# Performance work log

Hardware: AMD Instinct MI355X
Metric: run time of the kernel (lower is better)

The kernel has to match this reference:

```python
import jax, jax.numpy as jnp
import numpy as np

B, S, DM, H, D = 4, 2048, 1024, 16, 64
CAP = 15.0
EPS = 1e-6


def setup_inputs() -> dict:
    key = jax.random.key(0)
    ks = jax.random.split(key, 5)
    return {
        "x": jax.random.normal(ks[0], (B, S, DM), jnp.float32),
        "hidden_state": jnp.zeros((B, H, D, D), jnp.float32),
        "w_qkv": jax.random.normal(ks[1], (3 * H * D, DM), jnp.float32) * 0.02,
        "w_gate": jax.random.normal(ks[2], (3 * H, DM), jnp.float32) * 0.02,
        "w_out": jax.random.normal(ks[3], (DM, H * D), jnp.float32) * 0.02,
        "ln_w": jnp.ones((DM,), jnp.float32),
    }


def reference(x, hidden_state, w_qkv, w_gate, w_out, ln_w):
    Bq, Sq, DMq = x.shape
    residual = x
    # RMSNorm (computed in float32, matching the torch module)
    xf = x.astype(jnp.float32)
    var = jnp.mean(xf * xf, axis=-1, keepdims=True)
    xn = ln_w * (xf * jax.lax.rsqrt(var + EPS)).astype(x.dtype)
    # Fused qkv projection: (B,S,3,H,D)
    qkv = jnp.einsum('bsd,od->bso', xn, w_qkv).reshape(Bq, Sq, 3, H, D)
    q, k, v = qkv[:, :, 0], qkv[:, :, 1], qkv[:, :, 2]
    # Gates: (B,S,3,H) -> soft cap -> sigmoid
    gates = jnp.einsum('bsd,od->bso', xn, w_gate).reshape(Bq, Sq, 3, H)
    gates = jax.nn.sigmoid(CAP * jnp.tanh(gates / CAP))
    ig, fg, og = gates[:, :, 0], gates[:, :, 1], gates[:, :, 2]

    def step(h, inp):
        q_t, k_t, v_t, i_t, f_t, o_t = inp  # q/k/v: (B,H,D); gates: (B,H)
        kv = jnp.einsum('bhd,bhe->bhde', k_t, v_t)
        h = f_t[..., None, None] * h + i_t[..., None, None] * kv
        out = o_t[..., None] * jnp.einsum('bhd,bhde->bhe', q_t, h)
        return h, out

    xs = (q.swapaxes(0, 1), k.swapaxes(0, 1), v.swapaxes(0, 1),
          ig.swapaxes(0, 1), fg.swapaxes(0, 1), og.swapaxes(0, 1))
    h_final, outs = jax.lax.scan(step, hidden_state, xs)  # outs: (S,B,H,D)
    output = outs.swapaxes(0, 1).reshape(Bq, Sq, H * D)
    y = residual + output @ w_out.T
    return y, h_final
```

## Files before the change

### kernel.cpp

```cpp
#include <hip/hip_runtime.h>
#include <hip/hip_bf16.h>
#include <math.h>
#include <stdint.h>

#define Bq 4
#define Sq 2048
#define DMq 1024
#define Hq 16
#define Dq 64
#define CAPf 15.0f
#define EPSf 1e-6f
#define Tc 64
#define Cc (Sq / Tc)
#define QKVW (3 * Hq * Dq)

typedef __attribute__((ext_vector_type(8))) short short8;
typedef __attribute__((ext_vector_type(4))) float f32x4;
typedef __hip_bfloat16 bf16;

__device__ __forceinline__ float b2f(bf16 v) { return __bfloat162float(v); }
__device__ __forceinline__ bf16  f2b(float v) { return __float2bfloat16(v); }
__device__ __forceinline__ uint16_t f2bu(float f) {
    bf16 h = __float2bfloat16(f); uint16_t u; __builtin_memcpy(&u, &h, 2); return u;
}
__device__ __forceinline__ float bu2f(uint16_t u) {
    uint32_t x = ((uint32_t)u) << 16; float f; __builtin_memcpy(&f, &x, 4); return f;
}

__global__ void convert_f32_bf16(const float* __restrict__ in, bf16* __restrict__ out, int n4) {
    int i = blockIdx.x * 256 + threadIdx.x;
    if (i < n4) {
        float4 v = ((const float4*)in)[i];
        bf16 t[4] = {f2b(v.x), f2b(v.y), f2b(v.z), f2b(v.w)};
        ((uint2*)out)[i] = *(uint2*)t;
    }
}

__global__ void rmsnorm_kernel(const float* __restrict__ x,
                               const float* __restrict__ ln_w,
                               bf16* __restrict__ xn) {
    int row = blockIdx.x;
    const float4* xr = (const float4*)(x + (size_t)row * DMq);
    int tid = threadIdx.x;
    float4 v = xr[tid];
    float ss = v.x*v.x + v.y*v.y + v.z*v.z + v.w*v.w;
    #pragma unroll
    for (int off = 32; off > 0; off >>= 1) ss += __shfl_down(ss, off);
    __shared__ float red[4];
    int lane = tid & 63, wv = tid >> 6;
    if (lane == 0) red[wv] = ss;
    __syncthreads();
    float tot = red[0] + red[1] + red[2] + red[3];
    float rs = rsqrtf(tot * (1.0f / DMq) + EPSf);
    float4 w4 = ((const float4*)ln_w)[tid];
    bf16 t[4] = {f2b(v.x * rs * w4.x), f2b(v.y * rs * w4.y),
                 f2b(v.z * rs * w4.z), f2b(v.w * rs * w4.w)};
    *(uint2*)(xn + (size_t)row * DMq + tid * 4) = *(uint2*)t;
}

enum Epi { EPI_BF16 = 0, EPI_GATE = 1, EPI_RESID = 2 };

template<int EPI>
__global__ __launch_bounds__(256) void gemm_mfma(const bf16* __restrict__ A,
                                                 const bf16* __restrict__ Bw,
                                                 const float* __restrict__ resid,
                                                 void* __restrict__ Cv,
                                                 int M, int N, int K) {
    __shared__ bf16 As[128 * 64];
    __shared__ bf16 Bs[128 * 64];
    const int tid = threadIdx.x;
    const int w = tid >> 6;
    const int l = tid & 63;
    const int wr = (w >> 1) * 64;
    const int wc = (w & 1) * 64;
    const int bm = blockIdx.y * 128;
    const int bn = blockIdx.x * 128;

    const int lrow = l >> 3;
    const int swzc = ((l & 7) ^ lrow) * 8;

    const int fl = l & 15;
    const int kb = l >> 4;
    const int rsw = l & 7;

    f32x4 acc[4][4];
    #pragma unroll
    for (int i = 0; i < 4; i++)
        #pragma unroll
        for (int j = 0; j < 4; j++) acc[i][j] = (f32x4){0.f, 0.f, 0.f, 0.f};

    for (int k0 = 0; k0 < K; k0 += 64) {
        __syncthreads();
        #pragma unroll
        for (int inst = 0; inst < 4; inst++) {
            int r0 = w * 32 + inst * 8;
            const bf16* gp = A + (size_t)(bm + r0 + lrow) * K + k0 + swzc;
            __builtin_amdgcn_global_load_lds(
                (const __attribute__((address_space(1))) uint32_t*)gp,
                (__attribute__((address_space(3))) uint32_t*)(As + r0 * 64),
                16, 0, 0);
        }
        #pragma unroll
        for (int inst = 0; inst < 4; inst++) {
            int r0 = w * 32 + inst * 8;
            if (bn + r0 < N) {
                const bf16* gp = Bw + (size_t)(bn + r0 + lrow) * K + k0 + swzc;
                __builtin_amdgcn_global_load_lds(
                    (const __attribute__((address_space(1))) uint32_t*)gp,
                    (__attribute__((address_space(3))) uint32_t*)(Bs + r0 * 64),
                    16, 0, 0);
            }
        }
        __syncthreads();
        #pragma unroll
        for (int kk2 = 0; kk2 < 2; kk2++) {
            const int koff = (((kk2 << 2) + kb) ^ rsw) * 8;
            short8 af[4], bfr[4];
            #pragma unroll
            for (int i = 0; i < 4; i++)
                af[i] = *(const short8*)(As + (wr + i * 16 + fl) * 64 + koff);
            #pragma unroll
            for (int j = 0; j < 4; j++)
                bfr[j] = *(const short8*)(Bs + (wc + j * 16 + fl) * 64 + koff);
            #pragma unroll
            for (int i = 0; i < 4; i++)
                #pragma unroll
                for (int j = 0; j < 4; j++)
                    acc[i][j] = __builtin_amdgcn_mfma_f32_16x16x32_bf16(
                        af[i], bfr[j], acc[i][j], 0, 0, 0);
        }
    }

    #pragma unroll
    for (int i = 0; i < 4; i++) {
        #pragma unroll
        for (int j = 0; j < 4; j++) {
            int col = bn + wc + j * 16 + fl;
            if (EPI == EPI_GATE && col >= N) continue;
            #pragma unroll
            for (int r = 0; r < 4; r++) {
                int row = bm + wr + i * 16 + kb * 4 + r;
                size_t idx = (size_t)row * N + col;
                float v = acc[i][j][r];
                if (EPI == EPI_GATE) {
                    v = CAPf * tanhf(v * (1.0f / CAPf));
                    ((float*)Cv)[idx] = 1.0f / (1.0f + expf(-v));
                } else if (EPI == EPI_RESID) {
                    ((float*)Cv)[idx] = v + resid[idx];
                } else {
                    ((bf16*)Cv)[idx] = f2b(v);
                }
            }
        }
    }
}

__global__ __launch_bounds__(64) void chunk_intra(const bf16* __restrict__ qkvb,
                                                  const float* __restrict__ gates,
                                                  bf16* __restrict__ attb,
                                                  bf16* __restrict__ LT,
                                                  float* __restrict__ oaArr,
                                                  float* __restrict__ Fch) {
    const int blk = blockIdx.x;
    const int c  = blk & (Cc - 1);
    const int bh = blk >> 5;
    const int b = bh >> 4, hh = bh & 15;
    const int l = threadIdx.x;
    const int s0 = c * Tc;

    __shared__ bf16 KTs[4096];
    __shared__ bf16 VTs[4096];
    __shared__ bf16 Ps[4096];
    __shared__ float rowS[64], pcolS[64], wstS[64];

    const float* gp = gates + (size_t)(b * Sq + s0 + l) * (3 * Hq);
    float ig = gp[hh], fg = gp[Hq + hh], og = gp[2 * Hq + hh];
    float la = __logf(fg);
    #pragma unroll
    for (int off = 1; off < 64; off <<= 1) {
        float v = __shfl_up(la, off);
        if (l >= off) la += v;
    }
    float la63 = __shfl(la, 63);
    float li = __logf(ig);
    rowS[l]  = la + __logf(og);
    pcolS[l] = li - la;
    wstS[l]  = __expf(la63 - la + li);
    float oa = og * __expf(la);
    oaArr[(size_t)blk * 64 + l] = oa;
    if (l == 0) Fch[blk] = __expf(la63);
    __syncthreads();

    const int cg = l & 7, rp = l >> 3;
    const size_t rowBase = (size_t)(b * Sq + s0);
    const int kcol = (Hq + hh) * Dq, vcol = (2 * Hq + hh) * Dq;
    #pragma unroll
    for (int pass = 0; pass < 4; pass++) {
        int j0 = pass * 16 + rp * 2;
        const bf16* r0 = qkvb + (rowBase + j0) * QKVW;
        const bf16* r1 = qkvb + (rowBase + j0 + 1) * QKVW;
        short8 k0 = *(const short8*)(r0 + kcol + cg * 8);
        short8 k1 = *(const short8*)(r1 + kcol + cg * 8);
        short8 v0 = *(const short8*)(r0 + vcol + cg * 8);
        short8 v1 = *(const short8*)(r1 + vcol + cg * 8);
        float w0 = wstS[j0], w1 = wstS[j0 + 1];
        #pragma unroll
        for (int s = 0; s < 8; s++) {
            int cc = cg * 8 + s;
            int base = cc * 64 + ((((j0 >> 3) ^ (cc & 7) ^ (cc >> 3))) << 3) + (j0 & 7);
            uint32_t kp = (uint32_t)f2bu(bu2f((uint16_t)k0[s]) * w0)
                        | ((uint32_t)f2bu(bu2f((uint16_t)k1[s]) * w1) << 16);
            uint32_t vp = (uint32_t)(uint16_t)v0[s] | ((uint32_t)(uint16_t)v1[s] << 16);
            *(uint32_t*)&KTs[base] = kp;
            *(uint32_t*)&VTs[base] = vp;
        }
    }

    const int fl = l & 15, kb = l >> 4;
    const bf16* Qb = qkvb + rowBase * QKVW + hh * Dq;
    const bf16* Kb = qkvb + rowBase * QKVW + kcol;
    f32x4 accS[4][4];
    #pragma unroll
    for (int i = 0; i < 4; i++)
        #pragma unroll
        for (int j = 0; j < 4; j++) accS[i][j] = (f32x4){0.f, 0.f, 0.f, 0.f};
    #pragma unroll
    for (int ks = 0; ks < 2; ks++) {
        short8 qf[4], kf[4];
        #pragma unroll
        for (int i = 0; i < 4; i++)
            qf[i] = *(const short8*)(Qb + (size_t)(i * 16 + fl) * QKVW + ks * 32 + kb * 8);
        #pragma unroll
        for (int j = 0; j < 4; j++)
            kf[j] = *(const short8*)(Kb + (size_t)(j * 16 + fl) * QKVW + ks * 32 + kb * 8);
        #pragma unroll
        for (int i = 0; i < 4; i++)
            #pragma unroll
            for (int j = 0; j < 4; j++)
                accS[i][j] = __builtin_amdgcn_mfma_f32_16x16x32_bf16(qf[i], kf[j], accS[i][j], 0, 0, 0);
    }

    #pragma unroll
    for (int i = 0; i < 4; i++) {
        #pragma unroll
        for (int j = 0; j < 4; j++) {
            int jj = j * 16 + fl;
            float pc = pcolS[jj];
            #pragma unroll
            for (int r = 0; r < 4; r++) {
                int t = i * 16 + kb * 4 + r;
                float p = (jj <= t) ? __expf(rowS[t] + pc) * accS[i][j][r] : 0.f;
                int slot = (jj >> 3) ^ (t & 7) ^ (t >> 3);
                Ps[t * 64 + slot * 8 + (jj & 7)] = f2b(p);
            }
        }
    }
    __syncthreads();

    f32x4 accO[4][4], accL[4][4];
    #pragma unroll
    for (int i = 0; i < 4; i++)
        #pragma unroll
        for (int j = 0; j < 4; j++) {
            accO[i][j] = (f32x4){0.f, 0.f, 0.f, 0.f};
            accL[i][j] = (f32x4){0.f, 0.f, 0.f, 0.f};
        }
    #pragma unroll
    for (int ks = 0; ks < 2; ks++) {
        short8 pf[4], vt[4], kt[4];
        #pragma unroll
        for (int i = 0; i < 4; i++) {
            int row = i * 16 + fl;
            int koff = (((ks * 4 + kb) ^ (row & 7) ^ (row >> 3))) << 3;
            pf[i] = *(const short8*)(Ps  + row * 64 + koff);
            vt[i] = *(const short8*)(VTs + row * 64 + koff);
            kt[i] = *(const short8*)(KTs + row * 64 + koff);
        }
        #pragma unroll
        for (int i = 0; i < 4; i++)
            #pragma unroll
            for (int j = 0; j < 4; j++) {
                accO[i][j] = __builtin_amdgcn_mfma_f32_16x16x32_bf16(pf[i], vt[j], accO[i][j], 0, 0, 0);
                accL[i][j] = __builtin_amdgcn_mfma_f32_16x16x32_bf16(vt[i], kt[j], accL[i][j], 0, 0, 0);
            }
    }

    #pragma unroll
    for (int i = 0; i < 4; i++)
        #pragma unroll
        for (int j = 0; j < 4; j++)
            #pragma unroll
            for (int r = 0; r < 4; r++) {
                int rr = i * 16 + kb * 4 + r, cc2 = j * 16 + fl;
                attb[(rowBase + rr) * (Hq * Dq) + hh * Dq + cc2] = f2b(accO[i][j][r]);
                LT[(size_t)blk * 4096 + rr * 64 + cc2] = f2b(accL[i][j][r]);
            }
}

__global__ __launch_bounds__(256) void scan_pass2(bf16* __restrict__ LH,
                                                  const float* __restrict__ Fchunk,
                                                  const float* __restrict__ h0,
                                                  float* __restrict__ hfin) {
    int idx = blockIdx.x * 256 + threadIdx.x;
    int bh = idx >> 12;
    int ed = idx & 4095;
    int e = ed >> 6, d = ed & 63;
    float run = h0[(size_t)bh * 4096 + d * 64 + e];
    #pragma unroll
    for (int c = 0; c < Cc; c++) {
        float Fv = Fchunk[bh * Cc + c];
        size_t off = ((size_t)bh * Cc + c) * 4096 + ed;
        float Lv = b2f(LH[off]);
        LH[off] = f2b(run);
        run = Fv * run + Lv;
    }
    hfin[(size_t)bh * 4096 + d * 64 + e] = run;
}

__global__ __launch_bounds__(64) void chunk_cross(const bf16* __restrict__ qkvb,
                                                  const bf16* __restrict__ HT,
                                                  const float* __restrict__ oaArr,
                                                  bf16* __restrict__ attb) {
    const int blk = blockIdx.x;
    const int c = blk & (Cc - 1);
    const int bh = blk >> 5;
    const int b = bh >> 4, hh = bh & 15;
    const int l = threadIdx.x, fl = l & 15, kb = l >> 4;
    const size_t rowBase = (size_t)(b * Sq + c * Tc);
    __shared__ float oaS[64];
    oaS[l] = oaArr[(size_t)blk * 64 + l];
    __syncthreads();
    const bf16* Qb = qkvb + rowBase * QKVW + hh * Dq;
    const bf16* Hb = HT + (size_t)blk * 4096;
    f32x4 acc[4][4];
    #pragma unroll
    for (int i = 0; i < 4; i++)
        #pragma unroll
        for (int j = 0; j < 4; j++) acc[i][j] = (f32x4){0.f, 0.f, 0.f, 0.f};
    #pragma unroll
    for (int ks = 0; ks < 2; ks++) {
        short8 qf[4], hf[4];
        #pragma unroll
        for (int i = 0; i < 4; i++)
            qf[i] = *(const short8*)(Qb + (size_t)(i * 16 + fl) * QKVW + ks * 32 + kb * 8);
        #pragma unroll
        for (int j = 0; j < 4; j++)
            hf[j] = *(const short8*)(Hb + (j * 16 + fl) * 64 + ks * 32 + kb * 8);
        #pragma unroll
        for (int i = 0; i < 4; i++)
            #pragma unroll
            for (int j = 0; j < 4; j++)
                acc[i][j] = __builtin_amdgcn_mfma_f32_16x16x32_bf16(qf[i], hf[j], acc[i][j], 0, 0, 0);
    }
    #pragma unroll
    for (int i = 0; i < 4; i++)
        #pragma unroll
        for (int j = 0; j < 4; j++)
            #pragma unroll
            for (int r = 0; r < 4; r++) {
                int t = i * 16 + kb * 4 + r, e = j * 16 + fl;
                size_t idx = (rowBase + t) * (Hq * Dq) + hh * Dq + e;
                attb[idx] = f2b(b2f(attb[idx]) + oaS[t] * acc[i][j][r]);
            }
}

extern "C" void kernel_launch(void* const* d_in, const int* in_sizes, int n_in,
                              void* d_out, int out_size, void* d_ws, size_t ws_size,
                              hipStream_t stream) {
    const float* x      = (const float*)d_in[0];
    const float* h0     = (const float*)d_in[1];
    const float* w_qkv  = (const float*)d_in[2];
    const float* w_gate = (const float*)d_in[3];
    const float* w_out  = (const float*)d_in[4];
    const float* ln_w   = (const float*)d_in[5];

    const size_t MS = (size_t)Bq * Sq;
    const size_t BH = (size_t)Bq * Hq;

    float* p = (float*)d_ws;
    bf16*  xnb   = (bf16*)p;  p += MS * DMq / 2;
    bf16*  qkvb  = (bf16*)p;  p += MS * QKVW / 2;
    float* gates = p;         p += MS * 3 * Hq;
    float* oaArr = p;         p += BH * Cc * Tc;
    float* Fch   = p;         p += BH * Cc;
    bf16*  LT    = (bf16*)p;  p += BH * Cc * Dq * Dq / 2;
    bf16*  wqb   = (bf16*)p;  p += (size_t)QKVW * DMq / 2;
    bf16*  wgb   = (bf16*)p;  p += (size_t)3 * Hq * DMq / 2;
    bf16*  wob   = (bf16*)p;  p += (size_t)DMq * Hq * Dq / 2;
    size_t need = (size_t)(p - (float*)d_ws) * sizeof(float);
    if (ws_size < need) return;
    bf16* attb = xnb;

    float* y    = (float*)d_out;
    float* hfin = y + MS * DMq;

    convert_f32_bf16<<<dim3(3072), dim3(256), 0, stream>>>(w_qkv, wqb, QKVW * DMq / 4);
    convert_f32_bf16<<<dim3(48),   dim3(256), 0, stream>>>(w_gate, wgb, 3 * Hq * DMq / 4);
    convert_f32_bf16<<<dim3(1024), dim3(256), 0, stream>>>(w_out, wob, DMq * Hq * Dq / 4);

    rmsnorm_kernel<<<dim3(MS), dim3(256), 0, stream>>>(x, ln_w, xnb);

    gemm_mfma<EPI_BF16><<<dim3(QKVW / 128, MS / 128), dim3(256), 0, stream>>>(
        xnb, wqb, nullptr, qkvb, (int)MS, QKVW, DMq);

    gemm_mfma<EPI_GATE><<<dim3(1, MS / 128), dim3(256), 0, stream>>>(
        xnb, wgb, nullptr, gates, (int)MS, 3 * Hq, DMq);

    chunk_intra<<<dim3(BH * Cc), dim3(64), 0, stream>>>(qkvb, gates, attb, LT, oaArr, Fch);
    scan_pass2<<<dim3(BH * 4096 / 256), dim3(256), 0, stream>>>(LT, Fch, h0, hfin);
    chunk_cross<<<dim3(BH * Cc), dim3(64), 0, stream>>>(qkvb, LT, oaArr, attb);

    gemm_mfma<EPI_RESID><<<dim3(DMq / 128, MS / 128), dim3(256), 0, stream>>>(
        attb, wob, x, y, (int)MS, DMq, Hq * Dq);
}
```

Baseline: 177.1 us.

## Merge QKV and gate GEMMs into one double-buffered 256x256 tile kernel

Concatenates the gate weights onto the QKV weights (zero-padded to 3328 rows) so one GEMM produces both QKV and the gates, with the split epilogue picked per column. The new GEMM uses 256x256 tiles, 512 threads, double-buffered LDS staging that overlaps loads with MFMA, and setprio around the MFMA blocks. The three weight-conversion launches are folded into one kernel. It removes a separate poorly occupied gate GEMM and extra launches, at the cost of padded wasted columns, larger LDS/register use and a coarser grid.

```diff
diff --git a/kernel.cpp b/kernel.cpp
--- a/kernel.cpp
+++ b/kernel.cpp
@@ -13,6 +13,9 @@
 #define Tc 64
 #define Cc (Sq / Tc)
 #define QKVW (3 * Hq * Dq)
+#define NGATE (3 * Hq)
+#define NMERGE (QKVW + NGATE)
+#define NPAD 3328
 
 typedef __attribute__((ext_vector_type(8))) short short8;
 typedef __attribute__((ext_vector_type(4))) float f32x4;
@@ -27,12 +30,33 @@
     uint32_t x = ((uint32_t)u) << 16; float f; __builtin_memcpy(&f, &x, 4); return f;
 }
 
-__global__ void convert_f32_bf16(const float* __restrict__ in, bf16* __restrict__ out, int n4) {
+__global__ void convert_all(const float* __restrict__ wqkv,
+                            const float* __restrict__ wgate,
+                            const float* __restrict__ wout,
+                            bf16* __restrict__ wcomb, bf16* __restrict__ wob) {
+    const int n1 = QKVW * DMq / 4;
+    const int n2 = (NPAD - QKVW) * DMq / 4;
+    const int ng = NGATE * DMq / 4;
+    const int n3 = DMq * Hq * Dq / 4;
     int i = blockIdx.x * 256 + threadIdx.x;
-    if (i < n4) {
-        float4 v = ((const float4*)in)[i];
+    if (i < n1) {
+        float4 v = ((const float4*)wqkv)[i];
         bf16 t[4] = {f2b(v.x), f2b(v.y), f2b(v.z), f2b(v.w)};
-        ((uint2*)out)[i] = *(uint2*)t;
+        ((uint2*)wcomb)[i] = *(uint2*)t;
+    } else if (i < n1 + n2) {
+        int j = i - n1;
+        uint2 o = make_uint2(0u, 0u);
+        if (j < ng) {
+            float4 v = ((const float4*)wgate)[j];
+            bf16 t[4] = {f2b(v.x), f2b(v.y), f2b(v.z), f2b(v.w)};
+            o = *(uint2*)t;
+        }
+        ((uint2*)wcomb)[n1 + j] = o;
+    } else if (i < n1 + n2 + n3) {
+        int j = i - n1 - n2;
+        float4 v = ((const float4*)wout)[j];
+        bf16 t[4] = {f2b(v.x), f2b(v.y), f2b(v.z), f2b(v.w)};
+        ((uint2*)wob)[j] = *(uint2*)t;
     }
 }
 
@@ -58,14 +82,131 @@
     *(uint2*)(xn + (size_t)row * DMq + tid * 4) = *(uint2*)t;
 }
 
-enum Epi { EPI_BF16 = 0, EPI_GATE = 1, EPI_RESID = 2 };
-
-template<int EPI>
-__global__ __launch_bounds__(256) void gemm_mfma(const bf16* __restrict__ A,
-                                                 const bf16* __restrict__ Bw,
-                                                 const float* __restrict__ resid,
-                                                 void* __restrict__ Cv,
-                                                 int M, int N, int K) {
+__global__ __launch_bounds__(512, 2) void gemm_qkvgate(const bf16* __restrict__ A,
+                                                       const bf16* __restrict__ Bw,
+                                                       bf16* __restrict__ qkvb,
+                                                       float* __restrict__ gates) {
+    __shared__ bf16 lds[2][2][256 * 64];
+    const int tid = threadIdx.x;
+    const int w = tid >> 6;
+    const int l = tid & 63;
+    const int wrow = (w >> 2) * 128;
+    const int wcol = (w & 3) * 64;
+    const int bm = blockIdx.y * 256;
+    const int bn = blockIdx.x * 256;
+
+    const int lrow = l >> 3;
+    const int swzc = ((l & 7) ^ lrow) * 8;
+    const int fl = l & 15;
+    const int kb = l >> 4;
+    const int rsw = l & 7;
+
+    f32x4 acc[8][4];
+    #pragma unroll
+    for (int i = 0; i < 8; i++)
+        #pragma unroll
+        for (int j = 0; j < 4; j++) acc[i][j] = (f32x4){0.f, 0.f, 0.f, 0.f};
+
+    auto stage = [&](int slot, int kt) {
+        const int k0 = kt * 64;
+        #pragma unroll
+        for (int inst = 0; inst < 4; inst++) {
+            int r0 = w * 32 + inst * 8;
+            const bf16* gp = A + (size_t)(bm + r0 + lrow) * DMq + k0 + swzc;
+            __builtin_amdgcn_global_load_lds(
+                (const __attribute__((address_space(1))) uint32_t*)gp,
+                (__attribute__((address_space(3))) uint32_t*)(&lds[slot][0][r0 * 64]),
+                16, 0, 0);
+        }
+        #pragma unroll
+        for (int inst = 0; inst < 4; inst++) {
+            int r0 = w * 32 + inst * 8;
+            const bf16* gp = Bw + (size_t)(bn + r0 + lrow) * DMq + k0 + swzc;
+            __builtin_amdgcn_global_load_lds(
+                (const __attribute__((address_space(1))) uint32_t*)gp,
+                (__attribute__((address_space(3))) uint32_t*)(&lds[slot][1][r0 * 64]),
+                16, 0, 0);
+        }
+    };
+
+    auto compute_half = [&](int slot) {
+        const bf16* As_ = &lds[slot][0][0];
+        const bf16* Bs_ = &lds[slot][1][0];
+        short8 bfrag[4][2];
+        #pragma unroll
+        for (int j = 0; j < 4; j++)
+            #pragma unroll
+            for (int kk = 0; kk < 2; kk++) {
+                int row = wcol + j * 16 + fl;
+                bfrag[j][kk] = *(const short8*)(Bs_ + row * 64 + (((kk << 2) + kb) ^ rsw) * 8);
+            }
+        #pragma unroll
+        for (int q = 0; q < 4; q++) {
+            short8 af[2][2];
+            #pragma unroll
+            for (int ii = 0; ii < 2; ii++)
+                #pragma unroll
+                for (int kk = 0; kk < 2; kk++) {
+                    int row = wrow + (q * 2 + ii) * 16 + fl;
+                    af[ii][kk] = *(const short8*)(As_ + row * 64 + (((kk << 2) + kb) ^ rsw) * 8);
+                }
+            __builtin_amdgcn_s_setprio(1);
+            #pragma unroll
+            for (int ii = 0; ii < 2; ii++)
+                #pragma unroll
+                for (int j = 0; j < 4; j++)
+                    #pragma unroll
+                    for (int kk = 0; kk < 2; kk++)
+                        acc[q * 2 + ii][j] = __builtin_amdgcn_mfma_f32_16x16x32_bf16(
+                            af[ii][kk], bfrag[j][kk], acc[q * 2 + ii][j], 0, 0, 0);
+            __builtin_amdgcn_s_setprio(0);
+        }
+    };
+
+    stage(0, 0);
+    asm volatile("s_waitcnt vmcnt(0)" ::: "memory");
+    __builtin_amdgcn_s_barrier();
+    __builtin_amdgcn_sched_barrier(0);
+
+    #pragma unroll 1
+    for (int it = 0; it < 8; it++) {
+        stage(1, 2 * it + 1);
+        compute_half(0);
+        asm volatile("s_waitcnt vmcnt(0)" ::: "memory");
+        __builtin_amdgcn_s_barrier();
+        __builtin_amdgcn_sched_barrier(0);
+        if (it < 7) stage(0, 2 * it + 2);
+        compute_half(1);
+        asm volatile("s_waitcnt vmcnt(0)" ::: "memory");
+        __builtin_amdgcn_s_barrier();
+        __builtin_amdgcn_sched_barrier(0);
+    }
+
+    #pragma unroll
+    for (int i = 0; i < 8; i++) {
+        #pragma unroll
+        for (int j = 0; j < 4; j++) {
+            int col = bn + wcol + j * 16 + fl;
+            #pragma unroll
+            for (int r = 0; r < 4; r++) {
+                int row = bm + wrow + i * 16 + kb * 4 + r;
+                float v = acc[i][j][r];
+                if (col < QKVW) {
+                    qkvb[(size_t)row * QKVW + col] = f2b(v);
+                } else if (col < NMERGE) {
+                    float g = CAPf * tanhf(v * (1.0f / CAPf));
+                    gates[(size_t)row * NGATE + (col - QKVW)] = 1.0f / (1.0f + expf(-g));
+                }
+            }
+        }
+    }
+}
+
+__global__ __launch_bounds__(256) void gemm_out(const bf16* __restrict__ A,
+                                                const bf16* __restrict__ Bw,
+                                                const float* __restrict__ resid,
+                                                float* __restrict__ C,
+                                                int M, int N, int K) {
     __shared__ bf16 As[128 * 64];
     __shared__ bf16 Bs[128 * 64];
     const int tid = threadIdx.x;
@@ -78,7 +219,6 @@
 
     const int lrow = l >> 3;
     const int swzc = ((l & 7) ^ lrow) * 8;
-
     const int fl = l & 15;
     const int kb = l >> 4;
     const int rsw = l & 7;
@@ -103,13 +243,11 @@
         #pragma unroll
         for (int inst = 0; inst < 4; inst++) {
             int r0 = w * 32 + inst * 8;
-            if (bn + r0 < N) {
-                const bf16* gp = Bw + (size_t)(bn + r0 + lrow) * K + k0 + swzc;
-                __builtin_amdgcn_global_load_lds(
-                    (const __attribute__((address_space(1))) uint32_t*)gp,
-                    (__attribute__((address_space(3))) uint32_t*)(Bs + r0 * 64),
-                    16, 0, 0);
-            }
+            const bf16* gp = Bw + (size_t)(bn + r0 + lrow) * K + k0 + swzc;
+            __builtin_amdgcn_global_load_lds(
+                (const __attribute__((address_space(1))) uint32_t*)gp,
+                (__attribute__((address_space(3))) uint32_t*)(Bs + r0 * 64),
+                16, 0, 0);
         }
         __syncthreads();
         #pragma unroll
@@ -136,20 +274,11 @@
         #pragma unroll
         for (int j = 0; j < 4; j++) {
             int col = bn + wc + j * 16 + fl;
-            if (EPI == EPI_GATE && col >= N) continue;
             #pragma unroll
             for (int r = 0; r < 4; r++) {
                 int row = bm + wr + i * 16 + kb * 4 + r;
                 size_t idx = (size_t)row * N + col;
-                float v = acc[i][j][r];
-                if (EPI == EPI_GATE) {
-                    v = CAPf * tanhf(v * (1.0f / CAPf));
-                    ((float*)Cv)[idx] = 1.0f / (1.0f + expf(-v));
-                } else if (EPI == EPI_RESID) {
-                    ((float*)Cv)[idx] = v + resid[idx];
-                } else {
-                    ((bf16*)Cv)[idx] = f2b(v);
-                }
+                C[idx] = acc[i][j][r] + resid[idx];
             }
         }
     }
@@ -173,7 +302,7 @@
     __shared__ bf16 Ps[4096];
     __shared__ float rowS[64], pcolS[64], wstS[64];
 
-    const float* gp = gates + (size_t)(b * Sq + s0 + l) * (3 * Hq);
+    const float* gp = gates + (size_t)(b * Sq + s0 + l) * NGATE;
     float ig = gp[hh], fg = gp[Hq + hh], og = gp[2 * Hq + hh];
     float la = __logf(fg);
     #pragma unroll
@@ -380,12 +509,11 @@
     float* p = (float*)d_ws;
     bf16*  xnb   = (bf16*)p;  p += MS * DMq / 2;
     bf16*  qkvb  = (bf16*)p;  p += MS * QKVW / 2;
-    float* gates = p;         p += MS * 3 * Hq;
+    float* gates = p;         p += MS * NGATE;
     float* oaArr = p;         p += BH * Cc * Tc;
     float* Fch   = p;         p += BH * Cc;
     bf16*  LT    = (bf16*)p;  p += BH * Cc * Dq * Dq / 2;
-    bf16*  wqb   = (bf16*)p;  p += (size_t)QKVW * DMq / 2;
-    bf16*  wgb   = (bf16*)p;  p += (size_t)3 * Hq * DMq / 2;
+    bf16*  wcomb = (bf16*)p;  p += (size_t)NPAD * DMq / 2;
     bf16*  wob   = (bf16*)p;  p += (size_t)DMq * Hq * Dq / 2;
     size_t need = (size_t)(p - (float*)d_ws) * sizeof(float);
     if (ws_size < need) return;
@@ -394,22 +522,19 @@
     float* y    = (float*)d_out;
     float* hfin = y + MS * DMq;
 
-    convert_f32_bf16<<<dim3(3072), dim3(256), 0, stream>>>(w_qkv, wqb, QKVW * DMq / 4);
-    convert_f32_bf16<<<dim3(48),   dim3(256), 0, stream>>>(w_gate, wgb, 3 * Hq * DMq / 4);
-    convert_f32_bf16<<<dim3(1024), dim3(256), 0, stream>>>(w_out, wob, DMq * Hq * Dq / 4);
+    const int cvt_n = (QKVW * DMq + (NPAD - QKVW) * DMq + DMq * Hq * Dq) / 4;
+    convert_all<<<dim3((cvt_n + 255) / 256), dim3(256), 0, stream>>>(
+        w_qkv, w_gate, w_out, wcomb, wob);
 
     rmsnorm_kernel<<<dim3(MS), dim3(256), 0, stream>>>(x, ln_w, xnb);
 
-    gemm_mfma<EPI_BF16><<<dim3(QKVW / 128, MS / 128), dim3(256), 0, stream>>>(
-        xnb, wqb, nullptr, qkvb, (int)MS, QKVW, DMq);
-
-    gemm_mfma<EPI_GATE><<<dim3(1, MS / 128), dim3(256), 0, stream>>>(
-        xnb, wgb, nullptr, gates, (int)MS, 3 * Hq, DMq);
+    gemm_qkvgate<<<dim3(NPAD / 256, MS / 256), dim3(512), 0, stream>>>(
+        xnb, wcomb, qkvb, gates);
 
     chunk_intra<<<dim3(BH * Cc), dim3(64), 0, stream>>>(qkvb, gates, attb, LT, oaArr, Fch);
     scan_pass2<<<dim3(BH * 4096 / 256), dim3(256), 0, stream>>>(LT, Fch, h0, hfin);
     chunk_cross<<<dim3(BH * Cc), dim3(64), 0, stream>>>(qkvb, LT, oaArr, attb);
 
-    gemm_mfma<EPI_RESID><<<dim3(DMq / 128, MS / 128), dim3(256), 0, stream>>>(
+    gemm_out<<<dim3(DMq / 128, MS / 128), dim3(256), 0, stream>>>(
         attb, wob, x, y, (int)MS, DMq, Hq * Dq);
 }
```

Measured after the change: 187.3 us. +5.8%, slower.
